# Kernel tuning notes

Measured on AMD Instinct MI355X. Metric: run time of the kernel, lower is better.

Reference implementation:

```python
import jax, jax.numpy as jnp
import numpy as np

HEADS = 4
DIM_HEAD = 128


def setup_inputs() -> dict:
    key = jax.random.key(0)
    k1, k2, k3, k4 = jax.random.split(key, 4)
    b, dim, H, W = 4, 256, 128, 128
    hidden = HEADS * DIM_HEAD  # 512
    x = jax.random.normal(k1, (b, dim, H, W), dtype=jnp.float32)
    # 1x1 convs are pointwise matmuls over channels
    w_qkv = jax.random.normal(k2, (hidden * 3, dim), dtype=jnp.float32) * 0.02
    w_out = jax.random.normal(k3, (dim, hidden), dtype=jnp.float32) * 0.02
    b_out = jax.random.normal(k4, (dim,), dtype=jnp.float32) * 0.02
    return {"x": x, "w_qkv": w_qkv, "w_out": w_out, "b_out": b_out}


def reference(x, w_qkv, w_out, b_out):
    b, c, h, w = x.shape
    n = h * w
    # to_qkv: 1x1 conv (no bias) == channel matmul -> [b, 3*heads*dh, h, w]
    qkv = jnp.einsum('bchw,oc->bohw', x, w_qkv)
    # 'b (qkv heads d) h w -> qkv b heads d (h w)'
    qkv = qkv.reshape(b, 3, HEADS, DIM_HEAD, n)
    q, k, v = qkv[:, 0], qkv[:, 1], qkv[:, 2]  # each [b, heads, d, n]
    k = jax.nn.softmax(k, axis=-1)  # softmax over spatial positions
    context = jnp.einsum('bhdn,bhen->bhde', k, v)   # [b, heads, d, d]
    out = jnp.einsum('bhde,bhdn->bhen', context, q)  # [b, heads, d, n]
    out = out.reshape(b, HEADS * DIM_HEAD, h, w)
    # to_out: 1x1 conv with bias
    return jnp.einsum('bchw,oc->bohw', out, w_out) + b_out[None, :, None, None]
```

## Files before the change

kernel.cpp:

```cpp
#include <hip/hip_runtime.h>
#include <hip/hip_bf16.h>

#define HEADS 4
#define DH    128
#define CIN   256
#define NPIX  16384
#define NB    4
#define HID   512

typedef __attribute__((ext_vector_type(8))) short bf16x8;
typedef __attribute__((ext_vector_type(4))) float f32x4;
typedef __attribute__((ext_vector_type(2))) unsigned u32x2;

__device__ __forceinline__ unsigned short f2bfu(float f) {
    union { __hip_bfloat16 h; unsigned short u; } cv;
    cv.h = __float2bfloat16(f);
    return cv.u;
}
__device__ __forceinline__ float bf2f(unsigned short u) {
    return __uint_as_float(((unsigned)u) << 16);
}

typedef const __attribute__((address_space(1))) unsigned char* gas_t;
typedef __attribute__((address_space(3))) unsigned char* las_t;
__device__ __forceinline__ void glds16(const void* g, void* s) {
    __builtin_amdgcn_global_load_lds((gas_t)g, (las_t)s, 16, 0, 0);
}
__device__ __forceinline__ unsigned lds_off(const void* p) {
    return (unsigned)(size_t)(las_t)p;
}


__global__ __launch_bounds__(256) void xp_convert(const float* __restrict__ x,
                                                  unsigned short* __restrict__ xp)
{
    __shared__ float tile[64][67];
    const int b = blockIdx.z, c0 = blockIdx.y * 64, n0 = blockIdx.x * 64;
    const int t = threadIdx.x;
    const float* xb = x + ((size_t)b * CIN + c0) * NPIX + n0;
#pragma unroll
    for (int p = 0; p < 4; ++p) {
        const int c = p * 16 + (t >> 4);
        const int n = (t & 15) * 4;
        float4 v = *reinterpret_cast<const float4*>(xb + (size_t)c * NPIX + n);
        tile[c][n + 0] = v.x; tile[c][n + 1] = v.y;
        tile[c][n + 2] = v.z; tile[c][n + 3] = v.w;
    }
    __syncthreads();
    const int n16l = t >> 6, c16l = (t >> 4) & 3, n_loc = t & 15;
    unsigned short u16[16];
#pragma unroll
    for (int j = 0; j < 16; ++j)
        u16[j] = f2bfu(tile[c16l * 16 + j][n16l * 16 + n_loc]);
    unsigned short* dst = xp + (((size_t)(b * 1024 + (n0 >> 4) + n16l)) * 16
                                + (c0 >> 4) + c16l) * 256 + n_loc * 16;
    *reinterpret_cast<uint4*>(dst)     = *reinterpret_cast<const uint4*>(u16);
    *reinterpret_cast<uint4*>(dst + 8) = *reinterpret_cast<const uint4*>(u16 + 8);
}

__global__ __launch_bounds__(256) void wconv3(const float* __restrict__ w_qkv,
                                              const float* __restrict__ w_out,
                                              unsigned short* __restrict__ WkF,
                                              unsigned short* __restrict__ WvF,
                                              unsigned short* __restrict__ WqTF,
                                              unsigned short* __restrict__ WoF)
{
    const int t = threadIdx.x, lane = t & 63, wid = t >> 6;
    const int tile = blockIdx.x * 4 + wid;
    unsigned short u8[8];
    unsigned short* dst;
    if (tile < 256) {
        const int h = tile >> 6, d16 = (tile >> 3) & 7, c32 = tile & 7;
        const float* src = w_qkv + (size_t)(512 + h * 128 + d16 * 16 + (lane & 15)) * CIN
                         + c32 * 32 + (lane >> 4) * 8;
#pragma unroll
        for (int j = 0; j < 8; ++j) u8[j] = f2bfu(src[j]);
        dst = WkF + (size_t)tile * 512 + lane * 8;
    } else if (tile < 512) {
        const int t2 = tile - 256;
        const int h = t2 >> 6, e16 = (t2 >> 3) & 7, c32 = t2 & 7;
        const float* src = w_qkv + (size_t)(1024 + h * 128 + e16 * 16 + (lane & 15)) * CIN
                         + c32 * 32 + (lane >> 4) * 8;
#pragma unroll
        for (int j = 0; j < 8; ++j) u8[j] = f2bfu(src[j]);
        dst = WvF + (size_t)t2 * 512 + lane * 8;
    } else if (tile < 768) {
        const int t2 = tile - 512;
        const int h = t2 >> 6, c16 = (t2 >> 2) & 15, d32 = t2 & 3;
#pragma unroll
        for (int j = 0; j < 8; ++j)
            u8[j] = f2bfu(w_qkv[(size_t)(h * 128 + d32 * 32 + (lane >> 4) * 8 + j) * CIN
                                + c16 * 16 + (lane & 15)]);
        dst = WqTF + (size_t)t2 * 512 + lane * 8;
    } else {
        const int t2 = tile - 768;
        const int o16 = t2 >> 4, m32 = t2 & 15;
        const float* src = w_out + (size_t)(o16 * 16 + (lane & 15)) * HID
                         + m32 * 32 + (lane >> 4) * 8;
#pragma unroll
        for (int j = 0; j < 8; ++j) u8[j] = f2bfu(src[j]);
        dst = WoF + (size_t)t2 * 512 + lane * 8;
    }
    *reinterpret_cast<uint4*>(dst) = *reinterpret_cast<const uint4*>(u8);
}

__global__ __launch_bounds__(256, 2) void kg_fused8(const unsigned short* __restrict__ xp,
                                                    const unsigned short* __restrict__ WkF,
                                                    unsigned short* __restrict__ Gp,
                                                    float* __restrict__ S)
{
    __shared__ unsigned short sX[2][64 * 256];
    __shared__ unsigned short sP[8 * 512];

    const int wgid = blockIdx.x;
    const int xcd  = wgid & 7;
    const int k_   = wgid >> 3;
    const int hd   = k_ & 7;
    const int gg   = k_ >> 3;
    const int h = hd >> 1, dh = hd & 1;
    const int g = xcd + 8 * gg;
    const int ns = g & 15, b = g >> 4;
    const int bh = b * 4 + h;

    const int t = threadIdx.x, lane = t & 63, w = t >> 6;
    const int cl = lane & 15, q = lane >> 4, r0q = q * 4;
    const int boff = cl * 16 + (q & 1) * 8 + (q >> 1) * 256;
    const unsigned troff = (unsigned)((q >> 1) * 8192 + (q & 1) * 256 + cl * 8);

    bf16x8 aW[8];
#pragma unroll
    for (int ks = 0; ks < 8; ++ks)
        aW[ks] = *reinterpret_cast<const bf16x8*>(
            WkF + ((size_t)((h * 8 + dh * 4 + w) * 8 + ks)) * 512 + lane * 8);

    f32x4 accG[4][4] = {};
    float Sacc[4] = {};

    const unsigned short* xpb = xp + ((size_t)(b * 1024 + ns * 64) * 16) * 256;

#define STAGE(nt_, buf_)                                                        \
    {                                                                           \
        const unsigned short* src_ = xpb + (size_t)(nt_) * 16384;               \
        _Pragma("unroll")                                                       \
        for (int p = 0; p < 8; ++p)                                             \
            glds16(src_ + (size_t)p * 2048 + (size_t)t * 8,                     \
                   &sX[buf_][(size_t)p * 2048 + (size_t)w * 512]);              \
    }

    STAGE(0, 0);
    __syncthreads();

    int cur = 0;
    for (int nt = 0; nt < 16; ++nt) {
        if (nt < 15) STAGE(nt + 1, cur ^ 1);

        f32x4 acc1[4] = {};
#pragma unroll
        for (int ks = 0; ks < 8; ++ks) {
            bf16x8 bb[4];
#pragma unroll
            for (int fj = 0; fj < 4; ++fj)
                bb[fj] = *reinterpret_cast<const bf16x8*>(
                    &sX[cur][(fj * 16 + 2 * ks) * 256 + boff]);
#pragma unroll
            for (int fj = 0; fj < 4; ++fj)
                acc1[fj] = __builtin_amdgcn_mfma_f32_16x16x32_bf16(
                    aW[ks], bb[fj], acc1[fj], 0, 0, 0);
        }

#pragma unroll
        for (int fj = 0; fj < 4; ++fj)
#pragma unroll
            for (int r = 0; r < 4; ++r) {
                const float v = __expf(acc1[fj][r]);
                Sacc[r] += v;
                const int us = ((r0q + r) + 16 * ((fj & 1) * 2 + (cl >> 3))) * 8 + (cl & 7);
                sP[(w * 2 + (fj >> 1)) * 512 + us] = f2bfu(v);
            }
        __syncthreads();

        {
            const unsigned sx_base = lds_off(&sX[cur][0]);
#pragma unroll
            for (int kn = 0; kn < 2; ++kn) {
                u32x2 lo[4], hi[4];
#pragma unroll
                for (int fj = 0; fj < 4; ++fj) {
                    const int cc = w * 4 + fj;
                    const unsigned a = sx_base + (unsigned)((kn * 32 + cc) * 512) + troff;
                    asm volatile("ds_read_b64_tr_b16 %0, %2\n\t"
                                 "ds_read_b64_tr_b16 %1, %2 offset:128"
                                 : "=&v"(lo[fj]), "=&v"(hi[fj])
                                 : "v"(a));
                }
                asm volatile("s_waitcnt lgkmcnt(0)" ::: "memory");
                __builtin_amdgcn_sched_barrier(0);

                bf16x8 pa[4];
#pragma unroll
                for (int fi = 0; fi < 4; ++fi)
                    pa[fi] = *reinterpret_cast<const bf16x8*>(
                        &sP[(fi * 2 + kn) * 512 + lane * 8]);
#pragma unroll
                for (int fj = 0; fj < 4; ++fj) {
                    union { bf16x8 v; u32x2 h2[2]; } fb;
                    fb.h2[0] = lo[fj];
                    fb.h2[1] = hi[fj];
#pragma unroll
                    for (int fi = 0; fi < 4; ++fi)
                        accG[fi][fj] = __builtin_amdgcn_mfma_f32_16x16x32_bf16(
                            pa[fi], fb.v, accG[fi][fj], 0, 0, 0);
                }
            }
        }
        __syncthreads();
        cur ^= 1;
    }
#undef STAGE

#pragma unroll
    for (int r = 0; r < 4; ++r) {
        float v = Sacc[r];
        v += __shfl_xor(v, 1); v += __shfl_xor(v, 2);
        v += __shfl_xor(v, 4); v += __shfl_xor(v, 8);
        if (cl == 0)
            atomicAdd(&S[bh * 128 + dh * 64 + w * 16 + r0q + r], v);
    }

    unsigned short* gp = Gp + (size_t)(ns * 16 + bh) * 32768;
#pragma unroll
    for (int fi = 0; fi < 4; ++fi)
#pragma unroll
        for (int fj = 0; fj < 4; ++fj)
#pragma unroll
            for (int r = 0; r < 4; ++r)
                gp[(size_t)(dh * 64 + fi * 16 + r0q + r) * 256 + w * 64 + fj * 16 + cl]
                    = f2bfu(accG[fi][fj][r]);
}

__global__ __launch_bounds__(256) void g_reduce2(const unsigned short* __restrict__ Gp,
                                                 float* __restrict__ G)
{
    const int idx = blockIdx.x * 256 + threadIdx.x;
    const int bh = idx >> 15, dc = idx & 32767;
    float s = 0.f;
#pragma unroll
    for (int k = 0; k < 16; ++k)
        s += bf2f(Gp[((size_t)k * 16 + bh) * 32768 + dc]);
    G[idx] = s;
}

__global__ __launch_bounds__(256) void c1_kernel(const float* __restrict__ G,
                                                 const float* __restrict__ S,
                                                 const unsigned short* __restrict__ WvF,
                                                 const unsigned short* __restrict__ WqTF,
                                                 unsigned short* __restrict__ AbarF)
{
    __shared__ unsigned short sCtx[32 * 512];
    const int t = threadIdx.x, lane = t & 63, wid = t >> 6;
    const int bh = blockIdx.x, b = bh >> 2, h = bh & 3;
    const int cl = lane & 15, r0q = (lane >> 4) * 4;
    const int wr = wid >> 1, wc = wid & 1;
    const float* Gb = G + (size_t)bh * 32768;

    float invs[4];
#pragma unroll
    for (int fi = 0; fi < 4; ++fi)
        invs[fi] = 1.0f / S[bh * 128 + wr * 64 + fi * 16 + cl];

    f32x4 acc[4][4] = {};
#pragma unroll
    for (int ks = 0; ks < 8; ++ks) {
        bf16x8 a[4], bb[4];
#pragma unroll
        for (int fi = 0; fi < 4; ++fi) {
            const float* gp = Gb + (size_t)(wr * 64 + fi * 16 + cl) * 256
                            + ks * 32 + (lane >> 4) * 8;
            const float4 v0 = *reinterpret_cast<const float4*>(gp);
            const float4 v1 = *reinterpret_cast<const float4*>(gp + 4);
            unsigned short u8[8] = {
                f2bfu(v0.x * invs[fi]), f2bfu(v0.y * invs[fi]),
                f2bfu(v0.z * invs[fi]), f2bfu(v0.w * invs[fi]),
                f2bfu(v1.x * invs[fi]), f2bfu(v1.y * invs[fi]),
                f2bfu(v1.z * invs[fi]), f2bfu(v1.w * invs[fi]) };
            a[fi] = *reinterpret_cast<const bf16x8*>(u8);
        }
#pragma unroll
        for (int fj = 0; fj < 4; ++fj)
            bb[fj] = *reinterpret_cast<const bf16x8*>(
                WvF + ((size_t)(h * 8 + wc * 4 + fj) * 8 + ks) * 512 + lane * 8);
#pragma unroll
        for (int fi = 0; fi < 4; ++fi)
#pragma unroll
            for (int fj = 0; fj < 4; ++fj)
                acc[fi][fj] = __builtin_amdgcn_mfma_f32_16x16x32_bf16(
                    a[fi], bb[fj], acc[fi][fj], 0, 0, 0);
    }

#pragma unroll
    for (int fi = 0; fi < 4; ++fi)
#pragma unroll
        for (int fj = 0; fj < 4; ++fj)
#pragma unroll
            for (int r = 0; r < 4; ++r) {
                const int us = (cl + 16 * ((fi & 1) * 2 + ((r0q + r) >> 3))) * 8 + ((r0q + r) & 7);
                sCtx[((wc * 4 + fj) * 4 + wr * 2 + (fi >> 1)) * 512 + us] = f2bfu(acc[fi][fj][r]);
            }
    __syncthreads();

    const int we = wid >> 1, wcq = wid & 1;
    f32x4 acc2[4][8] = {};
#pragma unroll
    for (int ks = 0; ks < 4; ++ks) {
        bf16x8 a2[4], b2[8];
#pragma unroll
        for (int fi = 0; fi < 4; ++fi)
            a2[fi] = *reinterpret_cast<const bf16x8*>(
                &sCtx[((we * 4 + fi) * 4 + ks) * 512 + lane * 8]);
#pragma unroll
        for (int fj = 0; fj < 8; ++fj)
            b2[fj] = *reinterpret_cast<const bf16x8*>(
                WqTF + ((size_t)(h * 16 + wcq * 8 + fj) * 4 + ks) * 512 + lane * 8);
#pragma unroll
        for (int fi = 0; fi < 4; ++fi)
#pragma unroll
            for (int fj = 0; fj < 8; ++fj)
                acc2[fi][fj] = __builtin_amdgcn_mfma_f32_16x16x32_bf16(
                    a2[fi], b2[fj], acc2[fi][fj], 0, 0, 0);
    }

#pragma unroll
    for (int fi = 0; fi < 4; ++fi)
#pragma unroll
        for (int fj = 0; fj < 8; ++fj)
#pragma unroll
            for (int r = 0; r < 4; ++r) {
                const int c16 = wcq * 8 + fj;
                const int m32 = h * 4 + we * 2 + (fi >> 1);
                const int us  = (cl + 16 * ((fi & 1) * 2 + ((r0q + r) >> 3))) * 8 + ((r0q + r) & 7);
                AbarF[((size_t)(b * 16 + c16) * 16 + m32) * 512 + us] = f2bfu(acc2[fi][fj][r]);
            }
}

__global__ __launch_bounds__(256) void c2_kernel(const unsigned short* __restrict__ WoF,
                                                 const unsigned short* __restrict__ AbarF,
                                                 unsigned short* __restrict__ F2)
{
    const int t = threadIdx.x, lane = t & 63, wid = t >> 6;
    const int csp = blockIdx.x, b = blockIdx.y;
    const int cl = lane & 15, r0q = (lane >> 4) * 4;

    f32x4 acc[4][4] = {};
#pragma unroll
    for (int ks = 0; ks < 16; ++ks) {
        bf16x8 a[4], bb[4];
#pragma unroll
        for (int fi = 0; fi < 4; ++fi)
            a[fi] = *reinterpret_cast<const bf16x8*>(
                WoF + ((size_t)(wid * 4 + fi) * 16 + ks) * 512 + lane * 8);
#pragma unroll
        for (int fj = 0; fj < 4; ++fj)
            bb[fj] = *reinterpret_cast<const bf16x8*>(
                AbarF + ((size_t)(b * 16 + csp * 4 + fj) * 16 + ks) * 512 + lane * 8);
#pragma unroll
        for (int fi = 0; fi < 4; ++fi)
#pragma unroll
            for (int fj = 0; fj < 4; ++fj)
                acc[fi][fj] = __builtin_amdgcn_mfma_f32_16x16x32_bf16(
                    a[fi], bb[fj], acc[fi][fj], 0, 0, 0);
    }

#pragma unroll
    for (int fi = 0; fi < 4; ++fi)
#pragma unroll
        for (int fj = 0; fj < 4; ++fj)
#pragma unroll
            for (int r = 0; r < 4; ++r) {
                const int o16 = wid * 4 + fi;
                const int c32 = csp * 2 + (fj >> 1);
                const int us  = ((r0q + r) + 16 * ((fj & 1) * 2 + (cl >> 3))) * 8 + (cl & 7);
                F2[((size_t)(b * 16 + o16) * 8 + c32) * 512 + us] = f2bfu(acc[fi][fj][r]);
            }
}

__global__ __launch_bounds__(256, 2) void out_gemm4(const unsigned short* __restrict__ xp,
                                                    const unsigned short* __restrict__ F2,
                                                    const float* __restrict__ b_out,
                                                    float* __restrict__ out)
{
    __shared__ unsigned short sXT[128 * 256];
    const int t = threadIdx.x, lane = t & 63, wid = t >> 6;
    const int n0 = blockIdx.x * 128, m0 = blockIdx.y * 128, b = blockIdx.z;
    const int wr = wid >> 1, wc = wid & 1;
    const int cl = lane & 15, q = lane >> 4;
    const int boff = cl * 16 + (q & 1) * 8 + (q >> 1) * 256;

    const unsigned short* src = xp + ((size_t)(b * 1024 + (n0 >> 4)) * 16) * 256;
#pragma unroll
    for (int p = 0; p < 16; ++p)
        glds16(src + ((size_t)p * 256 + t) * 8, &sXT[((size_t)p * 256 + wid * 64) * 8]);
    __syncthreads();

    f32x4 acc[4][4] = {};
#pragma unroll
    for (int ks = 0; ks < 8; ++ks) {
        bf16x8 a[4], bb[4];
#pragma unroll
        for (int fi = 0; fi < 4; ++fi)
            a[fi] = *reinterpret_cast<const bf16x8*>(
                F2 + (((size_t)b * 16 + (m0 >> 4) + wr * 4 + fi) * 8 + ks) * 512 + lane * 8);
#pragma unroll
        for (int fj = 0; fj < 4; ++fj)
            bb[fj] = *reinterpret_cast<const bf16x8*>(
                &sXT[((wc * 4 + fj) * 16 + 2 * ks) * 256 + boff]);
#pragma unroll
        for (int fi = 0; fi < 4; ++fi)
#pragma unroll
            for (int fj = 0; fj < 4; ++fj)
                acc[fi][fj] = __builtin_amdgcn_mfma_f32_16x16x32_bf16(
                    a[fi], bb[fj], acc[fi][fj], 0, 0, 0);
    }

    const int r0q = q * 4;
#pragma unroll
    for (int fi = 0; fi < 4; ++fi)
#pragma unroll
        for (int r = 0; r < 4; ++r) {
            const int o = m0 + wr * 64 + fi * 16 + r0q + r;
            const float bias = b_out[o];
#pragma unroll
            for (int fj = 0; fj < 4; ++fj)
                out[((size_t)b * CIN + o) * NPIX + n0 + wc * 64 + fj * 16 + cl] =
                    acc[fi][fj][r] + bias;
        }
}

extern "C" void kernel_launch(void* const* d_in, const int* in_sizes, int n_in,
                              void* d_out, int out_size, void* d_ws, size_t ws_size,
                              hipStream_t stream)
{
    const float* x     = (const float*)d_in[0];
    const float* w_qkv = (const float*)d_in[1];
    const float* w_out = (const float*)d_in[2];
    const float* b_out = (const float*)d_in[3];
    float* out = (float*)d_out;

    char* ws = (char*)d_ws;
    unsigned short* xp    = (unsigned short*)ws;
    unsigned short* WkF   = (unsigned short*)(ws + (64ull << 20));
    unsigned short* WvF   = (unsigned short*)(ws + (64ull << 20) + (256u << 10));
    unsigned short* WqTF  = (unsigned short*)(ws + (64ull << 20) + (512u << 10));
    unsigned short* WoF   = (unsigned short*)(ws + (64ull << 20) + (768u << 10));
    float*          S     = (float*)(ws + (65ull << 20));
    float*          G     = (float*)(ws + (66ull << 20));
    unsigned short* AbarF = (unsigned short*)(ws + (68ull << 20));
    unsigned short* F2    = (unsigned short*)(ws + (69ull << 20));
    unsigned short* Gp    = (unsigned short*)(ws + (72ull << 20));

    hipMemsetAsync(S, 0, 2048 * sizeof(float), stream);
    xp_convert<<<dim3(NPIX / 64, CIN / 64, NB), 256, 0, stream>>>(x, xp);
    wconv3<<<256, 256, 0, stream>>>(w_qkv, w_out, WkF, WvF, WqTF, WoF);
    kg_fused8<<<512, 256, 0, stream>>>(xp, WkF, Gp, S);
    g_reduce2<<<2048, 256, 0, stream>>>(Gp, G);
    c1_kernel<<<16, 256, 0, stream>>>(G, S, WvF, WqTF, AbarF);
    c2_kernel<<<dim3(4, NB), 256, 0, stream>>>(WoF, AbarF, F2);
    out_gemm4<<<dim3(NPIX / 128, CIN / 128, NB), 256, 0, stream>>>(xp, F2, b_out, out);
}
```

Before: 121.9 us.

## Repartition context GEMM per wave to drop intra-iteration barrier

Each wave now computes only its own 16 rows of the partial context against all 256 columns, instead of a 4x4 fragment grid covering all rows. Because a wave then reads only the exp(K) tile it wrote to shared memory itself, the __syncthreads between the softmax write and the GEMM read is removed. The trade is that each wave now does four times as many transposed LDS reads of the X tile, and the wider lo/hi fragment arrays raise register pressure. The MFMA count is unchanged.

```diff
diff --git a/kernel.cpp b/kernel.cpp
--- a/kernel.cpp
+++ b/kernel.cpp
@@ -104,7 +104,7 @@
     *reinterpret_cast<uint4*>(dst) = *reinterpret_cast<const uint4*>(u8);
 }
 
-__global__ __launch_bounds__(256, 2) void kg_fused8(const unsigned short* __restrict__ xp,
+__global__ __launch_bounds__(256, 2) void kg_fused9(const unsigned short* __restrict__ xp,
                                                     const unsigned short* __restrict__ WkF,
                                                     unsigned short* __restrict__ Gp,
                                                     float* __restrict__ S)
@@ -133,7 +133,7 @@
         aW[ks] = *reinterpret_cast<const bf16x8*>(
             WkF + ((size_t)((h * 8 + dh * 4 + w) * 8 + ks)) * 512 + lane * 8);
 
-    f32x4 accG[4][4] = {};
+    f32x4 accG[16] = {};
     float Sacc[4] = {};
 
     const unsigned short* xpb = xp + ((size_t)(b * 1024 + ns * 64) * 16) * 256;
@@ -177,39 +177,31 @@
                 const int us = ((r0q + r) + 16 * ((fj & 1) * 2 + (cl >> 3))) * 8 + (cl & 7);
                 sP[(w * 2 + (fj >> 1)) * 512 + us] = f2bfu(v);
             }
-        __syncthreads();
 
         {
             const unsigned sx_base = lds_off(&sX[cur][0]);
 #pragma unroll
             for (int kn = 0; kn < 2; ++kn) {
-                u32x2 lo[4], hi[4];
-#pragma unroll
-                for (int fj = 0; fj < 4; ++fj) {
-                    const int cc = w * 4 + fj;
+                u32x2 lo[16], hi[16];
+#pragma unroll
+                for (int cc = 0; cc < 16; ++cc) {
                     const unsigned a = sx_base + (unsigned)((kn * 32 + cc) * 512) + troff;
                     asm volatile("ds_read_b64_tr_b16 %0, %2\n\t"
                                  "ds_read_b64_tr_b16 %1, %2 offset:128"
-                                 : "=&v"(lo[fj]), "=&v"(hi[fj])
+                                 : "=&v"(lo[cc]), "=&v"(hi[cc])
                                  : "v"(a));
                 }
+                const bf16x8 pa = *reinterpret_cast<const bf16x8*>(
+                    &sP[(w * 2 + kn) * 512 + lane * 8]);
                 asm volatile("s_waitcnt lgkmcnt(0)" ::: "memory");
                 __builtin_amdgcn_sched_barrier(0);
-
-                bf16x8 pa[4];
-#pragma unroll
-                for (int fi = 0; fi < 4; ++fi)
-                    pa[fi] = *reinterpret_cast<const bf16x8*>(
-                        &sP[(fi * 2 + kn) * 512 + lane * 8]);
-#pragma unroll
-                for (int fj = 0; fj < 4; ++fj) {
+#pragma unroll
+                for (int cc = 0; cc < 16; ++cc) {
                     union { bf16x8 v; u32x2 h2[2]; } fb;
-                    fb.h2[0] = lo[fj];
-                    fb.h2[1] = hi[fj];
-#pragma unroll
-                    for (int fi = 0; fi < 4; ++fi)
-                        accG[fi][fj] = __builtin_amdgcn_mfma_f32_16x16x32_bf16(
-                            pa[fi], fb.v, accG[fi][fj], 0, 0, 0);
+                    fb.h2[0] = lo[cc];
+                    fb.h2[1] = hi[cc];
+                    accG[cc] = __builtin_amdgcn_mfma_f32_16x16x32_bf16(
+                        pa, fb.v, accG[cc], 0, 0, 0);
                 }
             }
         }
@@ -229,13 +221,11 @@
 
     unsigned short* gp = Gp + (size_t)(ns * 16 + bh) * 32768;
 #pragma unroll
-    for (int fi = 0; fi < 4; ++fi)
-#pragma unroll
-        for (int fj = 0; fj < 4; ++fj)
-#pragma unroll
-            for (int r = 0; r < 4; ++r)
-                gp[(size_t)(dh * 64 + fi * 16 + r0q + r) * 256 + w * 64 + fj * 16 + cl]
-                    = f2bfu(accG[fi][fj][r]);
+    for (int cc = 0; cc < 16; ++cc)
+#pragma unroll
+        for (int r = 0; r < 4; ++r)
+            gp[(size_t)(dh * 64 + w * 16 + r0q + r) * 256 + cc * 16 + cl]
+                = f2bfu(accG[cc][r]);
 }
 
 __global__ __launch_bounds__(256) void g_reduce2(const unsigned short* __restrict__ Gp,
@@ -460,7 +450,7 @@
     hipMemsetAsync(S, 0, 2048 * sizeof(float), stream);
     xp_convert<<<dim3(NPIX / 64, CIN / 64, NB), 256, 0, stream>>>(x, xp);
     wconv3<<<256, 256, 0, stream>>>(w_qkv, w_out, WkF, WvF, WqTF, WoF);
-    kg_fused8<<<512, 256, 0, stream>>>(xp, WkF, Gp, S);
+    kg_fused9<<<512, 256, 0, stream>>>(xp, WkF, Gp, S);
     g_reduce2<<<2048, 256, 0, stream>>>(Gp, G);
     c1_kernel<<<16, 256, 0, stream>>>(G, S, WvF, WqTF, AbarF);
     c2_kernel<<<dim3(4, NB), 256, 0, stream>>>(WoF, AbarF, F2);
```

New measurement: 129.1 us. 1.06x slower.
